# Performance work log

Measured on AMD Instinct MI355X. Metric: run time of the kernel, lower is better.

Reference implementation:

```python
import math
import jax, jax.numpy as jnp
import numpy as np

D = 1024
B, L = 4, 4096


def _linear(x, W, b):
    # torch nn.Linear convention: y = x @ W.T + b, W: (out, in)
    return jnp.einsum('bld,ed->ble', x, W) + b


def _ma_k_activation(x, k=0.02):
    x = x / math.sqrt(x.shape[-1])
    return jax.nn.sigmoid(x * k)


def _ma_q_activation(x):
    x = -x / math.sqrt(x.shape[-1])
    return -jnp.where(x >= 0, x, 0.02 * x)  # -leaky_relu(x, 0.02)


def setup_inputs() -> dict:
    key = jax.random.key(0)
    ks = jax.random.split(key, 9)
    s = 1.0 / math.sqrt(D)
    return {
        'x': jax.random.normal(ks[0], (B, L, D), dtype=jnp.float32),
        'Wq1': jax.random.uniform(ks[1], (D, D), jnp.float32, -s, s),
        'bq1': jax.random.uniform(ks[2], (D,), jnp.float32, -s, s),
        'Wk1': jax.random.uniform(ks[3], (D, D), jnp.float32, -s, s),
        'bk1': jax.random.uniform(ks[4], (D,), jnp.float32, -s, s),
        'Wk2': jax.random.uniform(ks[5], (D, D), jnp.float32, -s, s),
        'bk2': jax.random.uniform(ks[6], (D,), jnp.float32, -s, s),
        'Wproj': jax.random.uniform(ks[7], (D, D), jnp.float32, -s, s),
        'bproj': jax.random.uniform(ks[8], (D,), jnp.float32, -s, s),
    }


def reference(x, Wq1, bq1, Wk1, bk1, Wk2, bk2, Wproj, bproj):
    V = x
    # AR branch: exponential keys, normalized running average, sigmoid query gate
    K = jnp.exp(_linear(x, Wk1, bk1))                      # (B,L,D)
    K_cum = jnp.cumsum(K, axis=1) + 1e-6
    S = jnp.cumsum(K * V, axis=1) / K_cum
    Q = jax.nn.sigmoid(_linear(x, Wq1, bq1))
    O_ar = S * Q
    # MA branch: residual errors gated by shifted (q,k) activations
    zero = jnp.zeros_like(x[:, :1, :])
    E = jnp.concatenate([zero, V[:, 1:, :] - O_ar[:, :-1, :]], axis=1)
    qk2_in = jnp.concatenate([zero, x[:, :-1, :]], axis=1)
    K2 = _ma_k_activation(_linear(qk2_in, Wk2, bk2))
    S2 = jnp.cumsum(K2 * E, axis=1)
    Q2 = _ma_q_activation(Q)
    Q2 = jnp.concatenate([zero, Q2[:, :-1, :]], axis=1)
    O_ma = S2 * Q2
    return _linear(O_ar + O_ma, Wproj, bproj)
```

## Files before the change

kernel.cpp:

```cpp
#include <hip/hip_runtime.h>

#define D_DIM 1024
#define L_DIM 4096
#define B_DIM 4
#define M_DIM (B_DIM * L_DIM)
#define N1    3072
#define CHUNKS 64
#define LC     64
#define KDIM  1024
#define NKT   16

using f32x4  = __attribute__((ext_vector_type(4))) float;
using bf16x8 = __attribute__((ext_vector_type(8))) short;

__device__ __forceinline__ unsigned short f2bf(float f) {
    unsigned u = __float_as_uint(f);
    u += 0x7fffu + ((u >> 16) & 1u);
    return (unsigned short)(u >> 16);
}
__device__ __forceinline__ float bf2f(unsigned short h) {
    return __uint_as_float(((unsigned)h) << 16);
}
__device__ __forceinline__ float sigmoidf_(float x) {
    return 1.0f / (1.0f + __expf(-x));
}

__global__ void cvt_bf16_kernel(const float* __restrict__ in, unsigned short* __restrict__ out, int n) {
    int i = (blockIdx.x * blockDim.x + threadIdx.x) * 4;
    if (i < n) {
        float4 v = *reinterpret_cast<const float4*>(in + i);
        uint2 p;
        p.x = (unsigned)f2bf(v.x) | ((unsigned)f2bf(v.y) << 16);
        p.y = (unsigned)f2bf(v.z) | ((unsigned)f2bf(v.w) << 16);
        *reinterpret_cast<uint2*>(out + i) = p;
    }
}

__device__ __forceinline__ void gld_lds16(const void* g, void* s) {
    __builtin_amdgcn_global_load_lds((const __attribute__((address_space(1))) void*)g,
                                     (__attribute__((address_space(3))) void*)s, 16, 0, 0);
}

#define BAR()  do { asm volatile("" ::: "memory"); __builtin_amdgcn_s_barrier(); asm volatile("" ::: "memory"); } while (0)
#define MFMA16(a_, b_, c_) __builtin_amdgcn_mfma_f32_16x16x32_bf16(a_, b_, c_, 0, 0, 0)

__global__ __launch_bounds__(512, 2) void gemm256(
        const unsigned short* __restrict__ A, const unsigned short* __restrict__ Bm,
        unsigned short* __restrict__ Cb, float* __restrict__ Cf,
        const float* __restrict__ bb0, const float* __restrict__ bb1, const float* __restrict__ bb2,
        int nwgDiv8, int mode) {
    extern __shared__ __align__(16) short lds[];
    const int tid  = threadIdx.x;
    const int wid  = tid >> 6, lane = tid & 63;
    const int wr   = wid >> 2, wc = wid & 3;
    const int lr   = lane & 15, kg = lane >> 4;

    int lin = blockIdx.y * 64 + blockIdx.x;
    int swz = (lin & 7) * nwgDiv8 + (lin >> 3);
    int bm = swz & 63;
    int bn = swz >> 6;
    const size_t rowA0 = (size_t)bm * 256;
    const size_t rowB0 = (size_t)bn * 256;

    const int rh = tid >> 2;
    const int sl = (tid & 3) ^ ((rh >> 1) & 3);
    const int wbase = (tid >> 6) * 512;
    const size_t aoffG = (size_t)rh * KDIM + sl * 8;

#define STAGE(Mp_, row0_, kt_, kh_, c_, mat_, cur_) \
    gld_lds16((Mp_) + ((row0_) + (size_t)(c_) * 128) * KDIM + (size_t)(kt_) * 64 + (kh_) * 32 + aoffG, \
              (void*)(lds + (cur_) * 32768 + (mat_) * 16384 + (kh_) * 8192 + (c_) * 4096 + wbase))

    const int slotR = kg ^ ((lr >> 1) & 3);
    const int aRd = (wr * 128 + lr) * 32 + slotR * 8;
    const int bRd = (wc * 64  + lr) * 32 + slotR * 8;

    f32x4 acc[8][4];
#pragma unroll
    for (int i = 0; i < 8; ++i)
#pragma unroll
        for (int j = 0; j < 4; ++j) acc[i][j] = (f32x4){0.f, 0.f, 0.f, 0.f};

    STAGE(A,  rowA0, 0, 0, 0, 0, 0); STAGE(A,  rowA0, 0, 0, 1, 0, 0);
    STAGE(Bm, rowB0, 0, 0, 0, 1, 0); STAGE(Bm, rowB0, 0, 0, 1, 1, 0);
    STAGE(A,  rowA0, 0, 1, 0, 0, 0); STAGE(A,  rowA0, 0, 1, 1, 0, 0);
    STAGE(Bm, rowB0, 0, 1, 0, 1, 0); STAGE(Bm, rowB0, 0, 1, 1, 1, 0);
    STAGE(A,  rowA0, 1, 0, 0, 0, 1); STAGE(A,  rowA0, 1, 0, 1, 0, 1);
    STAGE(Bm, rowB0, 1, 0, 0, 1, 1); STAGE(Bm, rowB0, 1, 0, 1, 1, 1);
    asm volatile("s_waitcnt vmcnt(4)" ::: "memory");
    BAR();

    for (int kt = 0; kt < NKT; ++kt) {
        const int cur = kt & 1;
        const short* A0 = lds + cur * 32768;
        const short* A1 = A0 + 8192;
        const short* B0 = A0 + 16384;
        const short* B1 = A0 + 24576;
        bf16x8 a[8], b0, b1, b2, b3;

        #pragma unroll
        for (int fm = 0; fm < 8; ++fm) a[fm] = *reinterpret_cast<const bf16x8*>(A0 + aRd + fm * 512);
        b0 = *reinterpret_cast<const bf16x8*>(B0 + bRd);
        b1 = *reinterpret_cast<const bf16x8*>(B0 + bRd + 512);
        b2 = *reinterpret_cast<const bf16x8*>(B0 + bRd + 1024);
        b3 = *reinterpret_cast<const bf16x8*>(B0 + bRd + 1536);
        if (kt + 1 < NKT) {
            const int nc = cur ^ 1;
            STAGE(A,  rowA0, kt + 1, 1, 0, 0, nc); STAGE(A,  rowA0, kt + 1, 1, 1, 0, nc);
            STAGE(Bm, rowB0, kt + 1, 1, 0, 1, nc); STAGE(Bm, rowB0, kt + 1, 1, 1, 1, nc);
        }
        BAR();
        __builtin_amdgcn_s_setprio(1);
        #pragma unroll
        for (int fm = 0; fm < 8; ++fm) {
            acc[fm][0] = MFMA16(b0, a[fm], acc[fm][0]);
            acc[fm][1] = MFMA16(b1, a[fm], acc[fm][1]);
        }
        __builtin_amdgcn_s_setprio(0);
        BAR();

        BAR();
        __builtin_amdgcn_s_setprio(1);
        #pragma unroll
        for (int fm = 0; fm < 8; ++fm) {
            acc[fm][2] = MFMA16(b2, a[fm], acc[fm][2]);
            acc[fm][3] = MFMA16(b3, a[fm], acc[fm][3]);
        }
        __builtin_amdgcn_s_setprio(0);
        BAR();

        #pragma unroll
        for (int fm = 0; fm < 8; ++fm) a[fm] = *reinterpret_cast<const bf16x8*>(A1 + aRd + fm * 512);
        b0 = *reinterpret_cast<const bf16x8*>(B1 + bRd);
        b1 = *reinterpret_cast<const bf16x8*>(B1 + bRd + 512);
        b2 = *reinterpret_cast<const bf16x8*>(B1 + bRd + 1024);
        b3 = *reinterpret_cast<const bf16x8*>(B1 + bRd + 1536);
        if (kt + 2 < NKT) {
            STAGE(A, rowA0, kt + 2, 0, 0, 0, cur); STAGE(A, rowA0, kt + 2, 0, 1, 0, cur);
        }
        BAR();
        __builtin_amdgcn_s_setprio(1);
        #pragma unroll
        for (int fm = 0; fm < 8; ++fm) {
            acc[fm][0] = MFMA16(b0, a[fm], acc[fm][0]);
            acc[fm][1] = MFMA16(b1, a[fm], acc[fm][1]);
        }
        __builtin_amdgcn_s_setprio(0);
        BAR();

        if (kt + 2 < NKT) {
            STAGE(Bm, rowB0, kt + 2, 0, 0, 1, cur); STAGE(Bm, rowB0, kt + 2, 0, 1, 1, cur);
        }
        BAR();
        __builtin_amdgcn_s_setprio(1);
        #pragma unroll
        for (int fm = 0; fm < 8; ++fm) {
            acc[fm][2] = MFMA16(b2, a[fm], acc[fm][2]);
            acc[fm][3] = MFMA16(b3, a[fm], acc[fm][3]);
        }
        __builtin_amdgcn_s_setprio(0);
        if (kt < NKT - 2) { asm volatile("s_waitcnt vmcnt(4)" ::: "memory"); }
        else              { asm volatile("s_waitcnt vmcnt(0)" ::: "memory"); }
        BAR();
    }

    const int rowBase = bm * 256 + wr * 128;
    const int colBase = bn * 256 + wc * 64;
    if (mode == 0) {
        const int seg = (colBase >> 10);
        const float* bs = (seg == 0) ? bb0 : ((seg == 1) ? bb1 : bb2);
#pragma unroll
        for (int fm = 0; fm < 8; ++fm) {
            int row = rowBase + fm * 16 + lr;
            unsigned short* cp = Cb + (size_t)row * 3072;
#pragma unroll
            for (int fn = 0; fn < 4; ++fn) {
                int col0 = colBase + fn * 16 + kg * 4;
                float4 b4 = *reinterpret_cast<const float4*>(bs + (col0 & 1023));
                float v0 = acc[fm][fn][0] + b4.x;
                float v1 = acc[fm][fn][1] + b4.y;
                float v2 = acc[fm][fn][2] + b4.z;
                float v3 = acc[fm][fn][3] + b4.w;
                float r0, r1, r2, r3;
                if (seg == 0)      { r0 = __expf(v0); r1 = __expf(v1); r2 = __expf(v2); r3 = __expf(v3); }
                else if (seg == 1) { r0 = sigmoidf_(v0); r1 = sigmoidf_(v1); r2 = sigmoidf_(v2); r3 = sigmoidf_(v3); }
                else               { r0 = sigmoidf_(v0 * 6.25e-4f); r1 = sigmoidf_(v1 * 6.25e-4f);
                                     r2 = sigmoidf_(v2 * 6.25e-4f); r3 = sigmoidf_(v3 * 6.25e-4f); }
                uint2 p;
                p.x = (unsigned)f2bf(r0) | ((unsigned)f2bf(r1) << 16);
                p.y = (unsigned)f2bf(r2) | ((unsigned)f2bf(r3) << 16);
                *reinterpret_cast<uint2*>(cp + col0) = p;
            }
        }
    } else {
#pragma unroll
        for (int fm = 0; fm < 8; ++fm) {
            int row = rowBase + fm * 16 + lr;
            float* cp = Cf + (size_t)row * 1024;
#pragma unroll
            for (int fn = 0; fn < 4; ++fn) {
                int col0 = colBase + fn * 16 + kg * 4;
                float4 b4 = *reinterpret_cast<const float4*>(bb0 + col0);
                float4 v;
                v.x = acc[fm][fn][0] + b4.x;
                v.y = acc[fm][fn][1] + b4.y;
                v.z = acc[fm][fn][2] + b4.z;
                v.w = acc[fm][fn][3] + b4.w;
                *reinterpret_cast<float4*>(cp + col0) = v;
            }
        }
    }
#undef STAGE
}

__global__ void pass1(const unsigned short* __restrict__ KQ, const float* __restrict__ x,
                      float* __restrict__ pK, float* __restrict__ pKV) {
    int tid = blockIdx.x * 256 + threadIdx.x;
    int d  = tid & 1023;
    int bc = tid >> 10;
    size_t row0 = ((size_t)(bc >> 6)) * L_DIM + (size_t)(bc & 63) * LC;
    const unsigned short* kp = KQ + row0 * 3072 + d;
    const float* vp = x + row0 * 1024 + d;
    float sK = 0.f, sKV = 0.f;
#pragma unroll 8
    for (int i = 0; i < LC; ++i) {
        float k = bf2f(kp[(size_t)i * 3072]);
        float v = vp[(size_t)i * 1024];
        sK += k;
        sKV += k * v;
    }
    pK[tid] = sK;
    pKV[tid] = sKV;
}

__global__ void scan_ex2(float* __restrict__ pK, float* __restrict__ pKV) {
    int tid = blockIdx.x * 256 + threadIdx.x;
    int d = tid & 1023, b = tid >> 10;
    float rK = 0.f, rKV = 0.f;
#pragma unroll 8
    for (int c = 0; c < CHUNKS; ++c) {
        size_t i = ((size_t)(b * CHUNKS + c)) * 1024 + d;
        float a = pK[i], q = pKV[i];
        pK[i] = rK; pKV[i] = rKV;
        rK += a; rKV += q;
    }
}

__global__ void scan_ex1(float* __restrict__ p) {
    int tid = blockIdx.x * 256 + threadIdx.x;
    int d = tid & 1023, b = tid >> 10;
    float r = 0.f;
#pragma unroll 8
    for (int c = 0; c < CHUNKS; ++c) {
        size_t i = ((size_t)(b * CHUNKS + c)) * 1024 + d;
        float a = p[i]; p[i] = r; r += a;
    }
}

__global__ void pass3(const unsigned short* __restrict__ KQ, const float* __restrict__ x,
                      const float* __restrict__ oK, const float* __restrict__ oKV,
                      unsigned short* __restrict__ oarB, unsigned short* __restrict__ mB,
                      float* __restrict__ pM) {
    int tid = blockIdx.x * 256 + threadIdx.x;
    int d  = tid & 1023;
    int bc = tid >> 10;
    int c  = bc & 63;
    size_t row0 = ((size_t)(bc >> 6)) * L_DIM + (size_t)c * LC;
    const unsigned short* kqp = KQ + row0 * 3072 + d;
    const float* vp = x + row0 * 1024 + d;
    float cK = oK[tid], cKV = oKV[tid];
    float oar_prev = 0.f;
    if (c != 0) {
        float qm1 = bf2f(kqp[-2048]);
        oar_prev = qm1 * (cKV / (cK + 1e-6f));
    }
    float sM = 0.f;
    {
        float k = bf2f(kqp[0]);
        float q = bf2f(kqp[1024]);
        float v = vp[0];
        cK += k; cKV += k * v;
        float oar = q * (cKV / (cK + 1e-6f));
        float m = 0.f;
        if (c != 0) {
            float k2 = bf2f(kqp[-1024]);
            m = k2 * (v - oar_prev);
        }
        sM += m;
        size_t gi = row0 * 1024 + d;
        oarB[gi] = f2bf(oar);
        mB[gi]   = f2bf(m);
        oar_prev = oar;
    }
#pragma unroll 4
    for (int i = 1; i < LC; ++i) {
        float k = bf2f(kqp[(size_t)i * 3072]);
        float q = bf2f(kqp[(size_t)i * 3072 + 1024]);
        float v = vp[(size_t)i * 1024];
        cK += k; cKV += k * v;
        float oar = q * (cKV / (cK + 1e-6f));
        float k2 = bf2f(kqp[(size_t)(i - 1) * 3072 + 2048]);
        float m = k2 * (v - oar_prev);
        sM += m;
        size_t gi = (row0 + (size_t)i) * 1024 + d;
        oarB[gi] = f2bf(oar);
        mB[gi]   = f2bf(m);
        oar_prev = oar;
    }
    pM[tid] = sM;
}

__global__ void pass5(const unsigned short* __restrict__ KQ,
                      const unsigned short* __restrict__ oarB, const unsigned short* __restrict__ mB,
                      const float* __restrict__ oM, unsigned short* __restrict__ yin) {
    int tid = blockIdx.x * 256 + threadIdx.x;
    int d  = tid & 1023;
    int bc = tid >> 10;
    int c  = bc & 63;
    size_t row0 = ((size_t)(bc >> 6)) * L_DIM + (size_t)c * LC;
    const unsigned short* qp = KQ + row0 * 3072 + 1024 + d;
    float cM = oM[tid];
    {
        size_t gi = row0 * 1024 + d;
        cM += bf2f(mB[gi]);
        float qm1 = (c == 0) ? 0.f : bf2f(qp[-3072]);
        yin[gi] = f2bf(bf2f(oarB[gi]) + cM * 6.25e-4f * qm1);
    }
#pragma unroll 4
    for (int i = 1; i < LC; ++i) {
        size_t gi = (row0 + (size_t)i) * 1024 + d;
        cM += bf2f(mB[gi]);
        float qm1 = bf2f(qp[(size_t)(i - 1) * 3072]);
        yin[gi] = f2bf(bf2f(oarB[gi]) + cM * 6.25e-4f * qm1);
    }
}

extern "C" void kernel_launch(void* const* d_in, const int* in_sizes, int n_in,
                              void* d_out, int out_size, void* d_ws, size_t ws_size,
                              hipStream_t stream) {
    (void)in_sizes; (void)n_in; (void)out_size; (void)ws_size;
    const float* x   = (const float*)d_in[0];
    const float* Wq1 = (const float*)d_in[1];
    const float* bq1 = (const float*)d_in[2];
    const float* Wk1 = (const float*)d_in[3];
    const float* bk1 = (const float*)d_in[4];
    const float* Wk2 = (const float*)d_in[5];
    const float* bk2 = (const float*)d_in[6];
    const float* Wpj = (const float*)d_in[7];
    const float* bpj = (const float*)d_in[8];
    float* out = (float*)d_out;

    char* ws = (char*)d_ws;
    unsigned short* xbf   = (unsigned short*)(ws);
    unsigned short* Wcat  = (unsigned short*)(ws + 33554432);
    unsigned short* Wpjbf = (unsigned short*)(ws + 39845888);
    unsigned short* KQ    = (unsigned short*)(ws + 41943040);
    unsigned short* oarB  = (unsigned short*)(ws + 142606336);
    unsigned short* mB    = (unsigned short*)(ws + 176160768);
    unsigned short* yin   = (unsigned short*)(ws + 209715200);
    float* pK  = (float*)(ws + 243269632);
    float* pKV = (float*)(ws + 244318208);
    float* pM  = (float*)(ws + 245366784);

    (void)hipFuncSetAttribute((const void*)gemm256,
                              hipFuncAttributeMaxDynamicSharedMemorySize, 131072);

    const int nx = M_DIM * D_DIM;
    const int nw = D_DIM * D_DIM;
    cvt_bf16_kernel<<<nx / 4 / 256, 256, 0, stream>>>(x, xbf, nx);
    cvt_bf16_kernel<<<nw / 4 / 256, 256, 0, stream>>>(Wk1, Wcat, nw);
    cvt_bf16_kernel<<<nw / 4 / 256, 256, 0, stream>>>(Wq1, Wcat + nw, nw);
    cvt_bf16_kernel<<<nw / 4 / 256, 256, 0, stream>>>(Wk2, Wcat + 2 * nw, nw);
    cvt_bf16_kernel<<<nw / 4 / 256, 256, 0, stream>>>(Wpj, Wpjbf, nw);

    gemm256<<<dim3(64, 12), 512, 131072, stream>>>(xbf, Wcat, KQ, nullptr,
                                                   bk1, bq1, bk2, 96, 0);

    pass1<<<M_DIM * D_DIM / LC / 256, 256, 0, stream>>>(KQ, x, pK, pKV);
    scan_ex2<<<16, 256, 0, stream>>>(pK, pKV);
    pass3<<<M_DIM * D_DIM / LC / 256, 256, 0, stream>>>(KQ, x, pK, pKV, oarB, mB, pM);
    scan_ex1<<<16, 256, 0, stream>>>(pM);
    pass5<<<M_DIM * D_DIM / LC / 256, 256, 0, stream>>>(KQ, oarB, mB, pM, yin);

    gemm256<<<dim3(64, 4), 512, 131072, stream>>>(yin, Wpjbf, nullptr, out,
                                                  bpj, nullptr, nullptr, 32, 1);
}
```

Baseline: 315.9 us.

## Fuse chunked scan passes into one decoupled-lookback kernel with LDS staging

Replaces the five-kernel chunked scan pipeline (pass1, two scan kernels, pass3, pass5) with a single kernel. Blocks take work in ticket order, publish their chunk partial sums with flag-tagged atomic stores, and wait on all earlier chunks' partials to form the prefix. The intermediate oar and m values stay in shared memory instead of round-tripping through global bf16 buffers, and V is read as bf16 rather than fp32. This removes launches and global traffic but adds spin-waiting, a serial lookback over up to 63 predecessors, and a memset. It also adds reduced precision on V.

```diff
diff --git a/kernel.cpp b/kernel.cpp
--- a/kernel.cpp
+++ b/kernel.cpp
@@ -5,8 +5,6 @@
 #define B_DIM 4
 #define M_DIM (B_DIM * L_DIM)
 #define N1    3072
-#define CHUNKS 64
-#define LC     64
 #define KDIM  1024
 #define NKT   16
 
@@ -213,125 +211,104 @@
 #undef STAGE
 }
 
-__global__ void pass1(const unsigned short* __restrict__ KQ, const float* __restrict__ x,
-                      float* __restrict__ pK, float* __restrict__ pKV) {
-    int tid = blockIdx.x * 256 + threadIdx.x;
-    int d  = tid & 1023;
-    int bc = tid >> 10;
-    size_t row0 = ((size_t)(bc >> 6)) * L_DIM + (size_t)(bc & 63) * LC;
-    const unsigned short* kp = KQ + row0 * 3072 + d;
-    const float* vp = x + row0 * 1024 + d;
+#define MARKV 0x5A5A5A5Au
+
+__device__ __forceinline__ void publish(unsigned long long* p, float v) {
+    unsigned long long w = ((unsigned long long)MARKV << 32) | (unsigned long long)__float_as_uint(v);
+    __hip_atomic_store(p, w, __ATOMIC_RELEASE, __HIP_MEMORY_SCOPE_AGENT);
+}
+__device__ __forceinline__ float waitval(unsigned long long* p) {
+    unsigned long long w = __hip_atomic_load(p, __ATOMIC_RELAXED, __HIP_MEMORY_SCOPE_AGENT);
+    while ((unsigned)(w >> 32) != MARKV) {
+        __builtin_amdgcn_s_sleep(4);
+        w = __hip_atomic_load(p, __ATOMIC_RELAXED, __HIP_MEMORY_SCOPE_AGENT);
+    }
+    return __uint_as_float((unsigned)w);
+}
+
+__global__ __launch_bounds__(256) void fused_scan(
+        const unsigned short* __restrict__ KQ, const unsigned short* __restrict__ xbf,
+        unsigned short* __restrict__ yin, unsigned long long* parts, unsigned* ticket) {
+    extern __shared__ unsigned short sm[];
+    unsigned short* oarS = sm;
+    unsigned short* mS   = sm + 16384;
+    __shared__ unsigned vsh;
+
+    const int thr = threadIdx.x;
+    if (thr == 0)
+        vsh = __hip_atomic_fetch_add(ticket, 1u, __ATOMIC_RELAXED, __HIP_MEMORY_SCOPE_AGENT);
+    __syncthreads();
+    const unsigned v = vsh;
+    const int c = v & 63, grp = v >> 6;
+    const int b = grp >> 2, dq = grp & 3;
+    const int d = dq * 256 + thr;
+    const size_t row0 = (size_t)b * L_DIM + (size_t)c * 64;
+    const unsigned short* kqp = KQ + row0 * 3072 + d;
+    const unsigned short* vp  = xbf + row0 * 1024 + d;
+
+    unsigned long long* pK  = parts;
+    unsigned long long* pKV = parts + 16 * 64 * 256;
+    unsigned long long* pM  = parts + 2 * 16 * 64 * 256;
+    const size_t slot = ((size_t)grp * 64 + c) * 256 + thr;
+
     float sK = 0.f, sKV = 0.f;
 #pragma unroll 8
-    for (int i = 0; i < LC; ++i) {
-        float k = bf2f(kp[(size_t)i * 3072]);
-        float v = vp[(size_t)i * 1024];
-        sK += k;
-        sKV += k * v;
-    }
-    pK[tid] = sK;
-    pKV[tid] = sKV;
-}
-
-__global__ void scan_ex2(float* __restrict__ pK, float* __restrict__ pKV) {
-    int tid = blockIdx.x * 256 + threadIdx.x;
-    int d = tid & 1023, b = tid >> 10;
-    float rK = 0.f, rKV = 0.f;
-#pragma unroll 8
-    for (int c = 0; c < CHUNKS; ++c) {
-        size_t i = ((size_t)(b * CHUNKS + c)) * 1024 + d;
-        float a = pK[i], q = pKV[i];
-        pK[i] = rK; pKV[i] = rKV;
-        rK += a; rKV += q;
-    }
-}
-
-__global__ void scan_ex1(float* __restrict__ p) {
-    int tid = blockIdx.x * 256 + threadIdx.x;
-    int d = tid & 1023, b = tid >> 10;
-    float r = 0.f;
-#pragma unroll 8
-    for (int c = 0; c < CHUNKS; ++c) {
-        size_t i = ((size_t)(b * CHUNKS + c)) * 1024 + d;
-        float a = p[i]; p[i] = r; r += a;
-    }
-}
-
-__global__ void pass3(const unsigned short* __restrict__ KQ, const float* __restrict__ x,
-                      const float* __restrict__ oK, const float* __restrict__ oKV,
-                      unsigned short* __restrict__ oarB, unsigned short* __restrict__ mB,
-                      float* __restrict__ pM) {
-    int tid = blockIdx.x * 256 + threadIdx.x;
-    int d  = tid & 1023;
-    int bc = tid >> 10;
-    int c  = bc & 63;
-    size_t row0 = ((size_t)(bc >> 6)) * L_DIM + (size_t)c * LC;
-    const unsigned short* kqp = KQ + row0 * 3072 + d;
-    const float* vp = x + row0 * 1024 + d;
-    float cK = oK[tid], cKV = oKV[tid];
-    float oar_prev = 0.f;
+    for (int t = 0; t < 64; ++t) {
+        float k = bf2f(kqp[(size_t)t * 3072]);
+        float w = bf2f(vp[(size_t)t * 1024]);
+        sK += k; sKV += k * w;
+    }
+    publish(&pK[slot], sK);
+    publish(&pKV[slot], sKV);
+
+    float offK = 0.f, offKV = 0.f;
+    for (int cp = 0; cp < c; ++cp) {
+        size_t s2 = ((size_t)grp * 64 + cp) * 256 + thr;
+        offK  += waitval(&pK[s2]);
+        offKV += waitval(&pKV[s2]);
+    }
+
+    float cK = offK, cKV = offKV;
+    float oar_prev = 0.f, k2_prev = 0.f;
     if (c != 0) {
-        float qm1 = bf2f(kqp[-2048]);
+        float qm1 = bf2f(kqp[-3072 + 1024]);
         oar_prev = qm1 * (cKV / (cK + 1e-6f));
+        k2_prev  = bf2f(kqp[-3072 + 2048]);
     }
     float sM = 0.f;
+#pragma unroll 4
+    for (int t = 0; t < 64; ++t) {
+        float k  = bf2f(kqp[(size_t)t * 3072]);
+        float q  = bf2f(kqp[(size_t)t * 3072 + 1024]);
+        float k2 = bf2f(kqp[(size_t)t * 3072 + 2048]);
+        float w  = bf2f(vp[(size_t)t * 1024]);
+        cK += k; cKV += k * w;
+        float oar = q * (cKV / (cK + 1e-6f));
+        float m = k2_prev * (w - oar_prev);
+        sM += m;
+        oarS[t * 256 + thr] = f2bf(oar);
+        mS[t * 256 + thr]   = f2bf(m);
+        oar_prev = oar; k2_prev = k2;
+    }
+    publish(&pM[slot], sM);
+
+    float offM = 0.f;
+    for (int cp = 0; cp < c; ++cp) {
+        size_t s2 = ((size_t)grp * 64 + cp) * 256 + thr;
+        offM += waitval(&pM[s2]);
+    }
+
+    float cM = offM;
     {
-        float k = bf2f(kqp[0]);
-        float q = bf2f(kqp[1024]);
-        float v = vp[0];
-        cK += k; cKV += k * v;
-        float oar = q * (cKV / (cK + 1e-6f));
-        float m = 0.f;
-        if (c != 0) {
-            float k2 = bf2f(kqp[-1024]);
-            m = k2 * (v - oar_prev);
-        }
-        sM += m;
-        size_t gi = row0 * 1024 + d;
-        oarB[gi] = f2bf(oar);
-        mB[gi]   = f2bf(m);
-        oar_prev = oar;
+        cM += bf2f(mS[thr]);
+        float qm1 = (c == 0) ? 0.f : bf2f(kqp[-3072 + 1024]);
+        yin[row0 * 1024 + d] = f2bf(bf2f(oarS[thr]) + cM * 6.25e-4f * qm1);
     }
 #pragma unroll 4
-    for (int i = 1; i < LC; ++i) {
-        float k = bf2f(kqp[(size_t)i * 3072]);
-        float q = bf2f(kqp[(size_t)i * 3072 + 1024]);
-        float v = vp[(size_t)i * 1024];
-        cK += k; cKV += k * v;
-        float oar = q * (cKV / (cK + 1e-6f));
-        float k2 = bf2f(kqp[(size_t)(i - 1) * 3072 + 2048]);
-        float m = k2 * (v - oar_prev);
-        sM += m;
-        size_t gi = (row0 + (size_t)i) * 1024 + d;
-        oarB[gi] = f2bf(oar);
-        mB[gi]   = f2bf(m);
-        oar_prev = oar;
-    }
-    pM[tid] = sM;
-}
-
-__global__ void pass5(const unsigned short* __restrict__ KQ,
-                      const unsigned short* __restrict__ oarB, const unsigned short* __restrict__ mB,
-                      const float* __restrict__ oM, unsigned short* __restrict__ yin) {
-    int tid = blockIdx.x * 256 + threadIdx.x;
-    int d  = tid & 1023;
-    int bc = tid >> 10;
-    int c  = bc & 63;
-    size_t row0 = ((size_t)(bc >> 6)) * L_DIM + (size_t)c * LC;
-    const unsigned short* qp = KQ + row0 * 3072 + 1024 + d;
-    float cM = oM[tid];
-    {
-        size_t gi = row0 * 1024 + d;
-        cM += bf2f(mB[gi]);
-        float qm1 = (c == 0) ? 0.f : bf2f(qp[-3072]);
-        yin[gi] = f2bf(bf2f(oarB[gi]) + cM * 6.25e-4f * qm1);
-    }
-#pragma unroll 4
-    for (int i = 1; i < LC; ++i) {
-        size_t gi = (row0 + (size_t)i) * 1024 + d;
-        cM += bf2f(mB[gi]);
-        float qm1 = bf2f(qp[(size_t)(i - 1) * 3072]);
-        yin[gi] = f2bf(bf2f(oarB[gi]) + cM * 6.25e-4f * qm1);
+    for (int t = 1; t < 64; ++t) {
+        cM += bf2f(mS[t * 256 + thr]);
+        float qm1 = bf2f(kqp[(size_t)(t - 1) * 3072 + 1024]);
+        yin[(row0 + (size_t)t) * 1024 + d] = f2bf(bf2f(oarS[t * 256 + thr]) + cM * 6.25e-4f * qm1);
     }
 }
 
@@ -355,15 +332,16 @@
     unsigned short* Wcat  = (unsigned short*)(ws + 33554432);
     unsigned short* Wpjbf = (unsigned short*)(ws + 39845888);
     unsigned short* KQ    = (unsigned short*)(ws + 41943040);
-    unsigned short* oarB  = (unsigned short*)(ws + 142606336);
-    unsigned short* mB    = (unsigned short*)(ws + 176160768);
-    unsigned short* yin   = (unsigned short*)(ws + 209715200);
-    float* pK  = (float*)(ws + 243269632);
-    float* pKV = (float*)(ws + 244318208);
-    float* pM  = (float*)(ws + 245366784);
+    unsigned short* yin   = (unsigned short*)(ws + 142606336);
+    unsigned long long* parts = (unsigned long long*)(ws + 176160768);
+    unsigned* ticket = (unsigned*)(ws + 182452224);
 
     (void)hipFuncSetAttribute((const void*)gemm256,
                               hipFuncAttributeMaxDynamicSharedMemorySize, 131072);
+    (void)hipFuncSetAttribute((const void*)fused_scan,
+                              hipFuncAttributeMaxDynamicSharedMemorySize, 65536);
+
+    (void)hipMemsetAsync(parts, 0, 6291456 + 64, stream);
 
     const int nx = M_DIM * D_DIM;
     const int nw = D_DIM * D_DIM;
@@ -376,11 +354,7 @@
     gemm256<<<dim3(64, 12), 512, 131072, stream>>>(xbf, Wcat, KQ, nullptr,
                                                    bk1, bq1, bk2, 96, 0);
 
-    pass1<<<M_DIM * D_DIM / LC / 256, 256, 0, stream>>>(KQ, x, pK, pKV);
-    scan_ex2<<<16, 256, 0, stream>>>(pK, pKV);
-    pass3<<<M_DIM * D_DIM / LC / 256, 256, 0, stream>>>(KQ, x, pK, pKV, oarB, mB, pM);
-    scan_ex1<<<16, 256, 0, stream>>>(pM);
-    pass5<<<M_DIM * D_DIM / LC / 256, 256, 0, stream>>>(KQ, oarB, mB, pM, yin);
+    fused_scan<<<1024, 256, 65536, stream>>>(KQ, xbf, yin, parts, ticket);
 
     gemm256<<<dim3(64, 4), 512, 131072, stream>>>(yin, Wpjbf, nullptr, out,
                                                   bpj, nullptr, nullptr, 32, 1);
```

Result: slower. 590.5 us (+86.9%).
